# Performance work log

Hardware: AMD Instinct MI355X
Metric: run time of the kernel (lower is better)

The kernel has to match this reference:

```python
import jax, jax.numpy as jnp
import numpy as np
import math

B, T, C, H = 4, 2048, 1024, 16
D = C // H  # head dim = 64


def setup_inputs() -> dict:
    key = jax.random.key(0)
    ks = jax.random.split(key, 5)
    scale = 0.02
    x = jax.random.normal(ks[0], (B, T, C), dtype=jnp.float32)
    # torch nn.Linear(n_embd, 3*n_embd): weight [3C, C]; we store transposed [C, 3C]
    W_kqv = jax.random.normal(ks[1], (C, 3 * C), dtype=jnp.float32) * scale
    b_kqv = jnp.zeros((3 * C,), dtype=jnp.float32)
    W_proj = jax.random.normal(ks[2], (C, C), dtype=jnp.float32) * scale
    b_proj = jnp.zeros((C,), dtype=jnp.float32)
    padding_mask = jnp.ones((B, T), dtype=jnp.int32)  # 1 = valid token
    return {"x": x, "W_kqv": W_kqv, "b_kqv": b_kqv, "W_proj": W_proj,
            "b_proj": b_proj, "padding_mask": padding_mask}


def reference(x, W_kqv, b_kqv, W_proj, b_proj, padding_mask):
    Bx, Tx, Cx = x.shape
    kqv = x @ W_kqv + b_kqv                      # [B,T,3C]
    # original splits as k, q, v (in that order)
    k, q, v = jnp.split(kqv, 3, axis=2)
    def heads(t):
        return t.reshape(Bx, Tx, H, D).transpose(0, 2, 1, 3)  # [B,H,T,D]
    k, q, v = heads(k), heads(q), heads(v)
    att = jnp.einsum('bhqd,bhkd->bhqk', q, k) * (1.0 / math.sqrt(D))  # [B,H,T,T]
    causal = jnp.tril(jnp.ones((Tx, Tx), dtype=bool))[None, None]     # [1,1,T,T]
    valid = causal & (padding_mask[:, None, None, :] != 0)            # [B,1,T,T] broadcast
    neg_inf = jnp.finfo(att.dtype).min
    att = jnp.where(valid, att, neg_inf)
    att = jax.nn.softmax(att, axis=-1)
    y = jnp.einsum('bhqk,bhkd->bhqd', att, v)    # [B,H,T,D]
    y = y.transpose(0, 2, 1, 3).reshape(Bx, Tx, Cx)
    return y @ W_proj + b_proj
```

## Files before the change

### kernel.cpp

```cpp
#include <hip/hip_runtime.h>


typedef short bf16x8 __attribute__((ext_vector_type(8)));
typedef float floatx4 __attribute__((ext_vector_type(4)));

#define MFMA16(a, b, c) __builtin_amdgcn_mfma_f32_16x16x32_bf16(a, b, c, 0, 0, 0)

#define ASYNC_COPY16(gp, lp)                                                   \
  __builtin_amdgcn_global_load_lds(                                            \
      (__attribute__((address_space(1))) void*)(gp),                           \
      (__attribute__((address_space(3))) void*)(lp), 16, 0, 0)

#define DRAIN_VMCNT() asm volatile("s_waitcnt vmcnt(0)" ::: "memory")

__device__ __forceinline__ short f2bf(float f) {
  union { float f; unsigned u; } c;
  c.f = f;
  unsigned r = c.u + 0x7fffu + ((c.u >> 16) & 1u);
  return (short)(r >> 16);
}

__global__ __launch_bounds__(256) void cvt_f32_bf16(const float* __restrict__ in,
                                                    short* __restrict__ out) {
  int i = (blockIdx.x * 256 + threadIdx.x) * 4;
  float4 v = *(const float4*)&in[i];
  short4 o;
  o.x = f2bf(v.x); o.y = f2bf(v.y); o.z = f2bf(v.z); o.w = f2bf(v.w);
  *(short4*)&out[i] = o;
}

__global__ __launch_bounds__(256) void pmb_kernel(const int* __restrict__ pm,
                                                  float* __restrict__ pmbf) {
  int i = blockIdx.x * 256 + threadIdx.x;
  pmbf[i] = pm[i] ? 0.0f : -1.0e38f;
}

__global__ __launch_bounds__(256) void transpose_cvt_tiled(const float* __restrict__ in,
                                                           short* __restrict__ out,
                                                           int N) {
  __shared__ float buf[64][65];
  const int t = threadIdx.x;
  const int k0 = blockIdx.y * 64, n0 = blockIdx.x * 64;
#pragma unroll
  for (int i = 0; i < 4; ++i) {
    int s = t + i * 256;
    int row = s >> 4, c4 = (s & 15) * 4;
    float4 v = *(const float4*)&in[(size_t)(k0 + row) * N + n0 + c4];
    buf[row][c4] = v.x; buf[row][c4 + 1] = v.y;
    buf[row][c4 + 2] = v.z; buf[row][c4 + 3] = v.w;
  }
  __syncthreads();
#pragma unroll
  for (int i = 0; i < 2; ++i) {
    int u = t + i * 256;
    int rn = u >> 3, ch = (u & 7) * 8;
    short tmp[8];
#pragma unroll
    for (int j = 0; j < 8; ++j) tmp[j] = f2bf(buf[ch + j][rn]);
    *(uint4*)&out[(size_t)(n0 + rn) * 1024 + k0 + ch] = *(uint4*)tmp;
  }
}

template <int MODE>
__global__ __launch_bounds__(256) void gemm_bt128(const short* __restrict__ A,
                                                  const short* __restrict__ Bt,
                                                  const float* __restrict__ bias,
                                                  void* __restrict__ Cout,
                                                  int M, int N, int K) {
  __shared__ short smem[128 * 136];
  short* As = smem;
  short* Bs = smem + 8192;
  const int tid = threadIdx.x;
  const int lane = tid & 63;
  const int wv = tid >> 6;
  const int l15 = lane & 15, quad = lane >> 4;
  const int xr = l15 & 7;
  const int m0 = blockIdx.y * 128, n0 = blockIdx.x * 128;
  const int wm = (wv >> 1) * 64, wn = (wv & 1) * 64;

  floatx4 acc[4][4] = {};

  const int srow = tid >> 3;
  const int gch = ((tid & 7) ^ (srow & 7)) * 8;

  const short* Ap = &A[(size_t)(m0 + srow) * K + gch];
  const short* Bp = &Bt[(size_t)(n0 + srow) * K + gch];
  short* Asp = &As[tid * 8];
  short* Bsp = &Bs[tid * 8];

  for (int k0 = 0; k0 < K; k0 += 64) {
#pragma unroll
    for (int i = 0; i < 4; ++i) {
      ASYNC_COPY16(Ap + (size_t)(i * 32) * K + k0, Asp + i * 2048);
      ASYNC_COPY16(Bp + (size_t)(i * 32) * K + k0, Bsp + i * 2048);
    }
    DRAIN_VMCNT();
    __syncthreads();
#pragma unroll
    for (int s = 0; s < 2; ++s) {
      const int chs = ((s * 4 + quad) ^ xr) * 8;
      bf16x8 af[4], bfr[4];
#pragma unroll
      for (int i = 0; i < 4; ++i) {
        af[i]  = *(const bf16x8*)&As[(wm + i * 16 + l15) * 64 + chs];
        bfr[i] = *(const bf16x8*)&Bs[(wn + i * 16 + l15) * 64 + chs];
      }
#pragma unroll
      for (int mi = 0; mi < 4; ++mi)
#pragma unroll
        for (int ni = 0; ni < 4; ++ni)
          acc[mi][ni] = MFMA16(af[mi], bfr[ni], acc[mi][ni]);
    }
    __syncthreads();
  }

  if (MODE == 0) {
    float* outf = (float*)Cout;
#pragma unroll
    for (int ni = 0; ni < 4; ++ni) {
      int col = n0 + wn + ni * 16 + l15;
      float bv = bias[col];
#pragma unroll
      for (int mi = 0; mi < 4; ++mi) {
#pragma unroll
        for (int rr = 0; rr < 4; ++rr) {
          int row = m0 + wm + mi * 16 + quad * 4 + rr;
          outf[(size_t)row * N + col] = acc[mi][ni][rr] + bv;
        }
      }
    }
  } else {
    short* outs = (short*)Cout;
    const size_t QOFF = (size_t)64 * 2048 * 64;
    const int sec = n0 >> 10;
#pragma unroll
    for (int ni = 0; ni < 4; ++ni) {
      int c = wn + ni * 16 + l15;
      float bv = bias[n0 + c];
#pragma unroll
      for (int mi = 0; mi < 4; ++mi) {
        int r0 = wm + mi * 16 + quad * 4;
#pragma unroll
        for (int rr = 0; rr < 4; ++rr) {
          short v = f2bf(acc[mi][ni][rr] + bv);
          if (sec < 2) smem[(r0 + rr) * 136 + c] = v;
          else         smem[c * 136 + (r0 + rr)] = v;
        }
      }
    }
    __syncthreads();
#pragma unroll
    for (int j = 0; j < 8; ++j) {
      int idx = j * 256 + tid;
      int rr2 = idx >> 4;
      int cc2 = (idx & 15) * 8;
      uint4 v = *(const uint4*)&smem[rr2 * 136 + cc2];
      if (sec < 2) {
        int colg = n0 + cc2;
        int hh = (colg >> 6) & 15, dd = colg & 63;
        int row = m0 + rr2, bb = row >> 11, tt = row & 2047;
        *(uint4*)(outs + (size_t)sec * QOFF +
                  (((size_t)(bb * 16 + hh) * 2048 + tt) * 64 + dd)) = v;
      } else {
        int colg = n0 + rr2;
        int hh = (colg >> 6) & 15, dd = colg & 63;
        int row = m0 + cc2, bb = row >> 11, tt = row & 2047;
        *(uint4*)(outs + 2 * QOFF +
                  ((size_t)(bb * 16 + hh) * 64 + dd) * 2048 + tt) = v;
      }
    }
  }
}

__global__ __launch_bounds__(256, 3) void attn_flash7(const short* __restrict__ Qd,
                                                      const short* __restrict__ Kd,
                                                      const short* __restrict__ Vd,
                                                      const float* __restrict__ pmbf,
                                                      short* __restrict__ y) {
  constexpr int T = 2048, C = 1024;
  __shared__ short Ks[128 * 64];
  __shared__ short Vs[64 * 128];
  __shared__ short Ps[4][32][64];

  const int tid = threadIdx.x;
  const int lane = tid & 63, w = tid >> 6;
  const int l15 = lane & 15, quad = lane >> 4;
  const int xr = l15 & 7;
  const int lin = blockIdx.x;
  const int qb = 15 - (lin >> 6);
  const int bh = lin & 63;
  const int b = bh >> 4, h = bh & 15;
  const short* Qb = Qd + (size_t)bh * T * 64;
  const short* Kb = Kd + (size_t)bh * T * 64;
  const short* Vb = Vd + (size_t)bh * 64 * T;
  const float* pmb = &pmbf[b * T];
  const int q0 = qb * 128;

  bf16x8 qf[2][2];
#pragma unroll
  for (int mi = 0; mi < 2; ++mi) {
    const short* qp = Qb + (size_t)(q0 + w * 32 + mi * 16 + l15) * 64;
    qf[mi][0] = *(const bf16x8*)&qp[quad * 8];
    qf[mi][1] = *(const bf16x8*)&qp[32 + quad * 8];
  }

  floatx4 Oacc[2][4] = {};
  float lpart[2][4] = {};

#pragma unroll 1
  for (int k0 = 0; k0 <= q0; k0 += 128) {
    {
      const short* ksrc = Kb + (size_t)k0 * 64;
      const short* vsrc = Vb + k0;
#pragma unroll
      for (int j = 0; j < 4; ++j) {
        int c = j * 256 + tid;
        int krow = c >> 3, kc = (c & 7) ^ (krow & 7);
        ASYNC_COPY16(ksrc + krow * 64 + kc * 8, &Ks[c * 8]);
        int vrow = c >> 4, vc = (c & 15) ^ (vrow & 7);
        ASYNC_COPY16(vsrc + (size_t)vrow * T + vc * 8, &Vs[c * 8]);
      }
    }
    DRAIN_VMCNT();
    __syncthreads();

    const bool diag = (k0 == q0);
    const float scale = 0.125f;

#pragma unroll
    for (int kh = 0; kh < 2; ++kh) {
      floatx4 Sacc[2][4] = {};
#pragma unroll
      for (int s = 0; s < 2; ++s) {
#pragma unroll
        for (int n4 = 0; n4 < 4; ++n4) {
          bf16x8 bK = *(const bf16x8*)
              &Ks[((kh * 4 + n4) * 16 + l15) * 64 + (((s * 4 + quad) ^ xr) * 8)];
          Sacc[0][n4] = MFMA16(qf[0][s], bK, Sacc[0][n4]);
          Sacc[1][n4] = MFMA16(qf[1][s], bK, Sacc[1][n4]);
        }
      }

      if (!diag) {
#pragma unroll
        for (int n4 = 0; n4 < 4; ++n4) {
          float pb = pmb[k0 + kh * 64 + n4 * 16 + l15];
          const int cb = n4 * 2 + (l15 >> 3);
#pragma unroll
          for (int mi = 0; mi < 2; ++mi)
#pragma unroll
            for (int rr = 0; rr < 4; ++rr) {
              float p = __expf(fmaf(Sacc[mi][n4][rr], scale, pb));
              lpart[mi][rr] += p;
              unsigned u = __builtin_bit_cast(unsigned, p);
              int prow = mi * 16 + quad * 4 + rr;
              Ps[w][prow][(cb ^ (prow & 7)) * 8 + (l15 & 7)] =
                  (short)((u + 0x8000u) >> 16);
            }
        }
      } else {
#pragma unroll
        for (int n4 = 0; n4 < 4; ++n4) {
          float pb = pmb[k0 + kh * 64 + n4 * 16 + l15];
          int colr = kh * 64 + n4 * 16 + l15;
          const int cb = n4 * 2 + (l15 >> 3);
#pragma unroll
          for (int mi = 0; mi < 2; ++mi) {
            int rowb = w * 32 + mi * 16 + quad * 4;
#pragma unroll
            for (int rr = 0; rr < 4; ++rr) {
              float p = __expf(fmaf(Sacc[mi][n4][rr], scale, pb));
              if (colr > rowb + rr) p = 0.f;
              lpart[mi][rr] += p;
              unsigned u = __builtin_bit_cast(unsigned, p);
              int prow = mi * 16 + quad * 4 + rr;
              Ps[w][prow][(cb ^ (prow & 7)) * 8 + (l15 & 7)] =
                  (short)((u + 0x8000u) >> 16);
            }
          }
        }
      }

#pragma unroll
      for (int ks2 = 0; ks2 < 2; ++ks2) {
        const int pco = (((ks2 * 4 + quad) ^ xr) * 8);
        bf16x8 ap0 = *(const bf16x8*)&Ps[w][l15][pco];
        bf16x8 ap1 = *(const bf16x8*)&Ps[w][16 + l15][pco];
#pragma unroll
        for (int nd = 0; nd < 4; ++nd) {
          bf16x8 bV = *(const bf16x8*)
              &Vs[(nd * 16 + l15) * 128 +
                  (((kh * 8 + ks2 * 4 + quad) ^ xr) * 8)];
          Oacc[0][nd] = MFMA16(ap0, bV, Oacc[0][nd]);
          Oacc[1][nd] = MFMA16(ap1, bV, Oacc[1][nd]);
        }
      }
    }
    __syncthreads();
  }

#pragma unroll
  for (int mi = 0; mi < 2; ++mi) {
    float inv_l[4];
#pragma unroll
    for (int rr = 0; rr < 4; ++rr) {
      float s = lpart[mi][rr];
#pragma unroll
      for (int d = 1; d < 16; d <<= 1) s += __shfl_xor(s, d, 64);
      inv_l[rr] = 1.0f / s;
    }
#pragma unroll
    for (int n = 0; n < 4; ++n) {
      int dcol = n * 16 + l15;
#pragma unroll
      for (int rr = 0; rr < 4; ++rr) {
        int rowq = q0 + w * 32 + mi * 16 + quad * 4 + rr;
        y[((size_t)(b * T + rowq)) * C + h * 64 + dcol] =
            f2bf(Oacc[mi][n][rr] * inv_l[rr]);
      }
    }
  }
}

extern "C" void kernel_launch(void* const* d_in, const int* in_sizes, int n_in,
                              void* d_out, int out_size, void* d_ws, size_t ws_size,
                              hipStream_t stream) {
  constexpr int B = 4, T = 2048, C = 1024;
  constexpr int M = B * T;
  constexpr int N1 = 3 * C;

  const float* x      = (const float*)d_in[0];
  const float* W_kqv  = (const float*)d_in[1];
  const float* b_kqv  = (const float*)d_in[2];
  const float* W_proj = (const float*)d_in[3];
  const float* b_proj = (const float*)d_in[4];
  const int*   pmask  = (const int*)d_in[5];
  float* out = (float*)d_out;

  const size_t QOFF = (size_t)64 * T * 64;

  short* xb     = (short*)d_ws;
  short* Wkqvt  = xb + (size_t)M * C;
  short* Wprojt = Wkqvt + (size_t)N1 * C;
  short* qkv    = Wprojt + (size_t)C * C;
  float* pmbf   = (float*)(qkv + 3 * QOFF);
  short* yb     = xb;

  short* Kd = qkv;
  short* Qd = qkv + QOFF;
  short* Vd = qkv + 2 * QOFF;

  cvt_f32_bf16<<<(M * C) / (256 * 4), 256, 0, stream>>>(x, xb);
  transpose_cvt_tiled<<<dim3(N1 / 64, 16), 256, 0, stream>>>(W_kqv, Wkqvt, N1);
  transpose_cvt_tiled<<<dim3(C / 64, 16), 256, 0, stream>>>(W_proj, Wprojt, C);
  pmb_kernel<<<(B * T) / 256, 256, 0, stream>>>(pmask, pmbf);

  gemm_bt128<2><<<dim3(N1 / 128, M / 128), 256, 0, stream>>>(xb, Wkqvt, b_kqv, Kd, M, N1, C);

  attn_flash7<<<dim3(1024), 256, 0, stream>>>(Qd, Kd, Vd, pmbf, yb);

  gemm_bt128<0><<<dim3(C / 128, M / 128), 256, 0, stream>>>(yb, Wprojt, b_proj, out, M, C, C);
}
```

Before: 256.1 us.

## Transpose score MFMA so each lane owns a query row, pack P stores

Swaps the MFMA operand order for QK^T so each lane holds four consecutive key columns of a single query row. That lets the P tile be written with one packed 8-byte LDS store per 4 values via v_cvt_pk_bf16_f32, instead of scalar 2-byte stores. The row-sum reduction shrinks from 4 values times 4 shuffles to one value with two shuffles plus a broadcast. The exp is also folded into a hardware exp2 with a log2e-scaled constant, and padding bias loads become float4. Risks include a changed rounding mode for the bf16 conversion and the new -3e38 bias interacting with exp2.

```diff
diff --git a/kernel.cpp b/kernel.cpp
--- a/kernel.cpp
+++ b/kernel.cpp
@@ -12,6 +12,15 @@
       (__attribute__((address_space(3))) void*)(lp), 16, 0, 0)
 
 #define DRAIN_VMCNT() asm volatile("s_waitcnt vmcnt(0)" ::: "memory")
+
+#if defined(__has_builtin)
+#if __has_builtin(__builtin_amdgcn_exp2f)
+#define EXP2(x) __builtin_amdgcn_exp2f(x)
+#endif
+#endif
+#ifndef EXP2
+#define EXP2(x) exp2f(x)
+#endif
 
 __device__ __forceinline__ short f2bf(float f) {
   union { float f; unsigned u; } c;
@@ -32,7 +41,7 @@
 __global__ __launch_bounds__(256) void pmb_kernel(const int* __restrict__ pm,
                                                   float* __restrict__ pmbf) {
   int i = blockIdx.x * 256 + threadIdx.x;
-  pmbf[i] = pm[i] ? 0.0f : -1.0e38f;
+  pmbf[i] = pm[i] ? 0.0f : -3.0e38f;
 }
 
 __global__ __launch_bounds__(256) void transpose_cvt_tiled(const float* __restrict__ in,
@@ -196,6 +205,8 @@
   const float* pmb = &pmbf[b * T];
   const int q0 = qb * 128;
 
+  const float SCALE2 = 0.18033688011112042f;
+
   bf16x8 qf[2][2];
 #pragma unroll
   for (int mi = 0; mi < 2; ++mi) {
@@ -205,7 +216,7 @@
   }
 
   floatx4 Oacc[2][4] = {};
-  float lpart[2][4] = {};
+  float lpart[2] = {};
 
 #pragma unroll 1
   for (int k0 = 0; k0 <= q0; k0 += 128) {
@@ -225,7 +236,6 @@
     __syncthreads();
 
     const bool diag = (k0 == q0);
-    const float scale = 0.125f;
 
 #pragma unroll
     for (int kh = 0; kh < 2; ++kh) {
@@ -236,47 +246,53 @@
         for (int n4 = 0; n4 < 4; ++n4) {
           bf16x8 bK = *(const bf16x8*)
               &Ks[((kh * 4 + n4) * 16 + l15) * 64 + (((s * 4 + quad) ^ xr) * 8)];
-          Sacc[0][n4] = MFMA16(qf[0][s], bK, Sacc[0][n4]);
-          Sacc[1][n4] = MFMA16(qf[1][s], bK, Sacc[1][n4]);
+          Sacc[0][n4] = MFMA16(bK, qf[0][s], Sacc[0][n4]);
+          Sacc[1][n4] = MFMA16(bK, qf[1][s], Sacc[1][n4]);
         }
       }
 
       if (!diag) {
 #pragma unroll
         for (int n4 = 0; n4 < 4; ++n4) {
-          float pb = pmb[k0 + kh * 64 + n4 * 16 + l15];
-          const int cb = n4 * 2 + (l15 >> 3);
-#pragma unroll
-          for (int mi = 0; mi < 2; ++mi)
+          floatx4 pb4 = *(const floatx4*)&pmb[k0 + kh * 64 + n4 * 16 + quad * 4];
+#pragma unroll
+          for (int mi = 0; mi < 2; ++mi) {
+            float p[4];
 #pragma unroll
             for (int rr = 0; rr < 4; ++rr) {
-              float p = __expf(fmaf(Sacc[mi][n4][rr], scale, pb));
-              lpart[mi][rr] += p;
-              unsigned u = __builtin_bit_cast(unsigned, p);
-              int prow = mi * 16 + quad * 4 + rr;
-              Ps[w][prow][(cb ^ (prow & 7)) * 8 + (l15 & 7)] =
-                  (short)((u + 0x8000u) >> 16);
+              p[rr] = EXP2(fmaf(Sacc[mi][n4][rr], SCALE2, pb4[rr]));
+              lpart[mi] += p[rr];
             }
+            unsigned lo, hi;
+            asm("v_cvt_pk_bf16_f32 %0, %1, %2" : "=v"(lo) : "v"(p[0]), "v"(p[1]));
+            asm("v_cvt_pk_bf16_f32 %0, %1, %2" : "=v"(hi) : "v"(p[2]), "v"(p[3]));
+            uint2 pk; pk.x = lo; pk.y = hi;
+            *(uint2*)&Ps[w][mi * 16 + l15]
+                        [((n4 * 2 + (quad >> 1)) ^ xr) * 8 + (quad & 1) * 4] = pk;
+          }
         }
       } else {
 #pragma unroll
         for (int n4 = 0; n4 < 4; ++n4) {
-          float pb = pmb[k0 + kh * 64 + n4 * 16 + l15];
-          int colr = kh * 64 + n4 * 16 + l15;
-          const int cb = n4 * 2 + (l15 >> 3);
+          floatx4 pb4 = *(const floatx4*)&pmb[k0 + kh * 64 + n4 * 16 + quad * 4];
+          const int colb = kh * 64 + n4 * 16 + quad * 4;
 #pragma unroll
           for (int mi = 0; mi < 2; ++mi) {
-            int rowb = w * 32 + mi * 16 + quad * 4;
+            const int rowb = w * 32 + mi * 16 + l15;
+            float p[4];
 #pragma unroll
             for (int rr = 0; rr < 4; ++rr) {
-              float p = __expf(fmaf(Sacc[mi][n4][rr], scale, pb));
-              if (colr > rowb + rr) p = 0.f;
-              lpart[mi][rr] += p;
-              unsigned u = __builtin_bit_cast(unsigned, p);
-              int prow = mi * 16 + quad * 4 + rr;
-              Ps[w][prow][(cb ^ (prow & 7)) * 8 + (l15 & 7)] =
-                  (short)((u + 0x8000u) >> 16);
+              float v = EXP2(fmaf(Sacc[mi][n4][rr], SCALE2, pb4[rr]));
+              if (colb + rr > rowb) v = 0.f;
+              p[rr] = v;
+              lpart[mi] += v;
             }
+            unsigned lo, hi;
+            asm("v_cvt_pk_bf16_f32 %0, %1, %2" : "=v"(lo) : "v"(p[0]), "v"(p[1]));
+            asm("v_cvt_pk_bf16_f32 %0, %1, %2" : "=v"(hi) : "v"(p[2]), "v"(p[3]));
+            uint2 pk; pk.x = lo; pk.y = hi;
+            *(uint2*)&Ps[w][mi * 16 + l15]
+                        [((n4 * 2 + (quad >> 1)) ^ xr) * 8 + (quad & 1) * 4] = pk;
           }
         }
       }
@@ -301,14 +317,13 @@
 
 #pragma unroll
   for (int mi = 0; mi < 2; ++mi) {
+    float s = lpart[mi];
+    s += __shfl_xor(s, 16, 64);
+    s += __shfl_xor(s, 32, 64);
     float inv_l[4];
 #pragma unroll
-    for (int rr = 0; rr < 4; ++rr) {
-      float s = lpart[mi][rr];
-#pragma unroll
-      for (int d = 1; d < 16; d <<= 1) s += __shfl_xor(s, d, 64);
-      inv_l[rr] = 1.0f / s;
-    }
+    for (int rr = 0; rr < 4; ++rr)
+      inv_l[rr] = 1.0f / __shfl(s, quad * 4 + rr, 16);
 #pragma unroll
     for (int n = 0; n < 4; ++n) {
       int dcol = n * 16 + l15;
```

Result: no change. 258.5 us (+0.9%).
